# Kernel optimization log

Measured on AMD Instinct MI355X. Metric: run time of the kernel, lower is better.

The kernel has to match this reference:

```python
import jax, jax.numpy as jnp
import numpy as np

HEAD_NUM = 8
NEG_BIG = 1e9  # additive mask constant from the original layer


def setup_inputs() -> dict:
    key = jax.random.key(0)
    ks = jax.random.split(key, 7)
    B, S, D = 4, 2048, 512
    return {
        "x": jax.random.normal(ks[0], (B, S, D), dtype=jnp.float32),
        "Wk": jax.random.normal(ks[1], (D, D), dtype=jnp.float32) * (1.0 / np.sqrt(D)),
        "bk": jax.random.normal(ks[2], (D,), dtype=jnp.float32) * 0.02,
        "Wv": jax.random.normal(ks[3], (D, D), dtype=jnp.float32) * (1.0 / np.sqrt(D)),
        "bv": jax.random.normal(ks[4], (D,), dtype=jnp.float32) * 0.02,
        "Wo": jax.random.normal(ks[5], (D, D), dtype=jnp.float32) * (1.0 / np.sqrt(D)),
        "bo": jax.random.normal(ks[6], (D,), dtype=jnp.float32) * 0.02,
    }


def reference(x, Wk, bk, Wv, bv, Wo, bo):
    B, S, D = x.shape
    H = HEAD_NUM
    hd = D // H
    # Original layer: query is NOT projected; key/value are.
    q = x
    k = x @ Wk + bk
    v = x @ Wv + bv
    # split heads: [B, H, S, hd]
    qh = q.reshape(B, S, H, hd).transpose(0, 2, 1, 3)
    kh = k.reshape(B, S, H, hd).transpose(0, 2, 1, 3)
    vh = v.reshape(B, S, H, hd).transpose(0, 2, 1, 3)
    # scaled dot-product scores [B, H, S, S] (normalized=True => 1/sqrt(head_dim))
    scale = 1.0 / jnp.sqrt(jnp.asarray(hd, dtype=x.dtype))
    e = jnp.einsum("bhqd,bhkd->bhqk", qh, kh) * scale
    # history_only=True => causal additive mask
    causal = jnp.tril(jnp.ones((S, S), dtype=x.dtype))
    e = e - (1.0 - causal) * NEG_BIG
    a = jax.nn.softmax(e, axis=-1)
    out = jnp.einsum("bhqk,bhkd->bhqd", a, vh)  # [B, H, S, hd]
    out = out.transpose(0, 2, 1, 3).reshape(B, S, D)
    return out @ Wo + bo
```

## Files before the change

kernel.cpp:

```cpp
#include <hip/hip_runtime.h>
#include <stdint.h>
#include <stddef.h>

typedef short bf16x8 __attribute__((ext_vector_type(8)));
typedef float f32x4 __attribute__((ext_vector_type(4)));
typedef int i32x4 __attribute__((ext_vector_type(4)));

#define AS1 __attribute__((address_space(1)))
#define AS3 __attribute__((address_space(3)))

#define KSCALE 0.18033688011112042f
#define MFMA16(A, B, C) __builtin_amdgcn_mfma_f32_16x16x32_bf16(A, B, C, 0, 0, 0)

__device__ __forceinline__ unsigned short f2bf(float f) {
    union { float f; uint32_t u; } v; v.f = f;
    return (unsigned short)((v.u + 0x7fffu + ((v.u >> 16) & 1u)) >> 16);
}

__global__ void prep(const float* __restrict__ x, const float* __restrict__ Wk,
                     const float* __restrict__ Wv, const float* __restrict__ Wo,
                     unsigned short* __restrict__ xb, unsigned short* __restrict__ WkvT,
                     unsigned short* __restrict__ WoT) {
    __shared__ float tile[32][33];
    const int bi = blockIdx.x;
    const int tid = threadIdx.x;
    if (bi < 4096) {
        int i = bi * 256 + tid;
        float4 v = reinterpret_cast<const float4*>(x)[i];
        ushort4 o;
        o.x = f2bf(v.x); o.y = f2bf(v.y); o.z = f2bf(v.z); o.w = f2bf(v.w);
        reinterpret_cast<ushort4*>(xb)[i] = o;
    } else {
        int j = bi - 4096;
        int z = j >> 8, rem = j & 255;
        int bk = (rem >> 4) * 32, bn = (rem & 15) * 32;
        const float* W = (z == 0) ? Wk : (z == 1) ? Wv : Wo;
        unsigned short* WT = (z == 2) ? WoT : (WkvT + (size_t)z * 512 * 512);
        int tx = tid & 31, ty = tid >> 5;
#pragma unroll
        for (int r = 0; r < 32; r += 8)
            tile[ty + r][tx] = W[(size_t)(bk + ty + r) * 512 + bn + tx];
        __syncthreads();
#pragma unroll
        for (int r = 0; r < 32; r += 8)
            WT[(size_t)(bn + ty + r) * 512 + bk + tx] = f2bf(tile[tx][ty + r]);
    }
}

__global__ __launch_bounds__(256, 2) void gemmKV(const unsigned short* __restrict__ A,
                                                 const unsigned short* __restrict__ BT,
                                                 const float* __restrict__ bk,
                                                 const float* __restrict__ bv,
                                                 unsigned short* __restrict__ kbuf,
                                                 unsigned short* __restrict__ vTb) {
    __shared__ unsigned short lA[64 * 64];
    __shared__ unsigned short lB[128 * 64];
    const int tid = threadIdx.x;
    const int tile_n = blockIdx.x * 128;
    const int tile_m = blockIdx.y * 64;
    const int wid = tid >> 6, lane = tid & 63;
    const int wm = (wid >> 1) * 32, wn = (wid & 1) * 64;
    const int l16 = lane & 15, lg = lane >> 4;

    f32x4 acc[2][4];
#pragma unroll
    for (int i = 0; i < 2; ++i)
#pragma unroll
        for (int j = 0; j < 4; ++j)
            acc[i][j] = (f32x4){0.f, 0.f, 0.f, 0.f};

    const int r0 = tid >> 3;
    const int cr = tid & 7;

    for (int kt = 0; kt < 512; kt += 64) {
#pragma unroll
        for (int i = 0; i < 2; ++i) {
            int r = r0 + i * 32;
            int crs = cr ^ (r & 7);
            __builtin_amdgcn_global_load_lds((const AS1 void*)(A + (size_t)(tile_m + r) * 512 + kt + crs * 8),
                                             (AS3 void*)(&lA[(i * 256 + tid) * 8]), 16, 0, 0);
        }
#pragma unroll
        for (int i = 0; i < 4; ++i) {
            int r = r0 + i * 32;
            int crs = cr ^ (r & 7);
            __builtin_amdgcn_global_load_lds((const AS1 void*)(BT + (size_t)(tile_n + r) * 512 + kt + crs * 8),
                                             (AS3 void*)(&lB[(i * 256 + tid) * 8]), 16, 0, 0);
        }
        __syncthreads();
#pragma unroll
        for (int ks = 0; ks < 2; ++ks) {
            bf16x8 af[2], bfr[4];
#pragma unroll
            for (int f = 0; f < 2; ++f) {
                int ra = wm + f * 16 + l16;
                af[f] = *reinterpret_cast<const bf16x8*>(
                    reinterpret_cast<const char*>(lA) + ra * 128 + (((ks * 4 + lg) ^ (ra & 7)) << 4));
            }
#pragma unroll
            for (int f = 0; f < 4; ++f) {
                int rb = wn + f * 16 + l16;
                bfr[f] = *reinterpret_cast<const bf16x8*>(
                    reinterpret_cast<const char*>(lB) + rb * 128 + (((ks * 4 + lg) ^ (rb & 7)) << 4));
            }
#pragma unroll
            for (int fm = 0; fm < 2; ++fm)
#pragma unroll
                for (int fn = 0; fn < 4; ++fn)
                    acc[fm][fn] = MFMA16(af[fm], bfr[fn], acc[fm][fn]);
        }
        __syncthreads();
    }

#pragma unroll
    for (int fm = 0; fm < 2; ++fm)
#pragma unroll
        for (int fn = 0; fn < 4; ++fn) {
            int gm0 = tile_m + wm + fm * 16 + lg * 4;
            int gn = tile_n + wn + fn * 16 + l16;
            bool isK = gn < 512;
            int gnn = isK ? gn : gn - 512;
            float bs = isK ? bk[gnn] : bv[gnn];
            int hh = gnn >> 6, d = gnn & 63;
#pragma unroll
            for (int r = 0; r < 4; ++r) {
                float v = acc[fm][fn][r] + bs;
                int m = gm0 + r;
                int b = m >> 11, s = m & 2047;
                if (isK)
                    kbuf[(((size_t)(b * 8 + hh) * 2048 + s) << 6) + d] = f2bf(v * KSCALE);
                else
                    vTb[(((size_t)(b * 8 + hh) * 64 + d) << 11) + s] = f2bf(v);
            }
        }
}

__global__ __launch_bounds__(256, 2) void gemmO(const unsigned short* __restrict__ A,
                                                const unsigned short* __restrict__ BT,
                                                const float* __restrict__ bias,
                                                float* __restrict__ outp) {
    __shared__ unsigned short lA[64 * 64];
    __shared__ unsigned short lB[128 * 64];
    const int tid = threadIdx.x;
    const int tile_n = blockIdx.x * 128;
    const int tile_m = blockIdx.y * 64;
    const int wid = tid >> 6, lane = tid & 63;
    const int wm = (wid >> 1) * 32, wn = (wid & 1) * 64;
    const int l16 = lane & 15, lg = lane >> 4;

    f32x4 acc[2][4];
#pragma unroll
    for (int i = 0; i < 2; ++i)
#pragma unroll
        for (int j = 0; j < 4; ++j)
            acc[i][j] = (f32x4){0.f, 0.f, 0.f, 0.f};

    const int r0 = tid >> 3;
    const int cr = tid & 7;

    for (int kt = 0; kt < 512; kt += 64) {
#pragma unroll
        for (int i = 0; i < 2; ++i) {
            int r = r0 + i * 32;
            int crs = cr ^ (r & 7);
            __builtin_amdgcn_global_load_lds((const AS1 void*)(A + (size_t)(tile_m + r) * 512 + kt + crs * 8),
                                             (AS3 void*)(&lA[(i * 256 + tid) * 8]), 16, 0, 0);
        }
#pragma unroll
        for (int i = 0; i < 4; ++i) {
            int r = r0 + i * 32;
            int crs = cr ^ (r & 7);
            __builtin_amdgcn_global_load_lds((const AS1 void*)(BT + (size_t)(tile_n + r) * 512 + kt + crs * 8),
                                             (AS3 void*)(&lB[(i * 256 + tid) * 8]), 16, 0, 0);
        }
        __syncthreads();
#pragma unroll
        for (int ks = 0; ks < 2; ++ks) {
            bf16x8 af[2], bfr[4];
#pragma unroll
            for (int f = 0; f < 2; ++f) {
                int ra = wm + f * 16 + l16;
                af[f] = *reinterpret_cast<const bf16x8*>(
                    reinterpret_cast<const char*>(lA) + ra * 128 + (((ks * 4 + lg) ^ (ra & 7)) << 4));
            }
#pragma unroll
            for (int f = 0; f < 4; ++f) {
                int rb = wn + f * 16 + l16;
                bfr[f] = *reinterpret_cast<const bf16x8*>(
                    reinterpret_cast<const char*>(lB) + rb * 128 + (((ks * 4 + lg) ^ (rb & 7)) << 4));
            }
#pragma unroll
            for (int fm = 0; fm < 2; ++fm)
#pragma unroll
                for (int fn = 0; fn < 4; ++fn)
                    acc[fm][fn] = MFMA16(af[fm], bfr[fn], acc[fm][fn]);
        }
        __syncthreads();
    }

#pragma unroll
    for (int fm = 0; fm < 2; ++fm)
#pragma unroll
        for (int fn = 0; fn < 4; ++fn) {
            int gm0 = tile_m + wm + fm * 16 + lg * 4;
            int gn = tile_n + wn + fn * 16 + l16;
            float bs = bias[gn];
#pragma unroll
            for (int r = 0; r < 4; ++r)
                outp[(size_t)(gm0 + r) * 512 + gn] = acc[fm][fn][r] + bs;
        }
}

__global__ __launch_bounds__(256, 3) void attn_f(const unsigned short* __restrict__ xq,
                                                 const unsigned short* __restrict__ kg,
                                                 const unsigned short* __restrict__ vT,
                                                 unsigned short* __restrict__ ob) {
    __shared__ unsigned short lsK[3][4096];
    __shared__ unsigned short lsV[3][4096];

    const int tid = threadIdx.x;
    const int lane = tid & 63;
    const int w = tid >> 6;
    const int l16 = lane & 15, lg = lane >> 4;
    const int bh = blockIdx.x, b = bh >> 3, h = bh & 7;
    const int qblk = 31 - blockIdx.y;
    const int qlo = qblk * 64 + w * 16;
    const int q = qlo + l16;

    const unsigned short* Kb = kg + (size_t)bh * (2048 * 64);
    const unsigned short* Vb = vT + (size_t)bh * (64 * 2048);

    const unsigned short* qp = xq + ((size_t)(b * 2048 + qlo + l16) * 512) + h * 64 + lg * 8;
    bf16x8 qf0 = *(const bf16x8*)qp;
    bf16x8 qf1 = *(const bf16x8*)(qp + 32);

    f32x4 o[4];
#pragma unroll
    for (int i = 0; i < 4; ++i) o[i] = (f32x4){0.f, 0.f, 0.f, 0.f};
    float lsum = 0.f;

    const int nph = qblk + 1;

    const int srow = tid >> 3;
    const int scs = (tid & 7) ^ (srow & 7);
    const int skey = 8 * ((srow >> 2) & 3) + (srow & 3) + 4 * (srow >> 4);

#define STAGE(B, PH) { \
        const int kv0_ = (PH) << 6; \
        __builtin_amdgcn_global_load_lds((const AS1 void*)(Kb + (size_t)(kv0_ + skey) * 64 + scs * 8), \
            (AS3 void*)(&lsK[B][(size_t)tid * 8]), 16, 0, 0); \
        __builtin_amdgcn_global_load_lds((const AS1 void*)(Kb + (size_t)(kv0_ + 32 + skey) * 64 + scs * 8), \
            (AS3 void*)(&lsK[B][(size_t)(256 + tid) * 8]), 16, 0, 0); \
        __builtin_amdgcn_global_load_lds((const AS1 void*)(Vb + (size_t)srow * 2048 + kv0_ + scs * 8), \
            (AS3 void*)(&lsV[B][(size_t)tid * 8]), 16, 0, 0); \
        __builtin_amdgcn_global_load_lds((const AS1 void*)(Vb + (size_t)(srow + 32) * 2048 + kv0_ + scs * 8), \
            (AS3 void*)(&lsV[B][(size_t)(256 + tid) * 8]), 16, 0, 0); }

#define QKGRP(G, PA, PB, KS, KVB) { \
            const char* r0p = (KS) + (32 * (G) + l16) * 128; \
            const char* r1p = r0p + 16 * 128; \
            bf16x8 k00 = *(const bf16x8*)(r0p + ((lg ^ sw) << 4)); \
            bf16x8 k01 = *(const bf16x8*)(r0p + (((lg + 4) ^ sw) << 4)); \
            bf16x8 k10 = *(const bf16x8*)(r1p + ((lg ^ sw) << 4)); \
            bf16x8 k11 = *(const bf16x8*)(r1p + (((lg + 4) ^ sw) << 4)); \
            f32x4 sA = (f32x4){0.f,0.f,0.f,0.f}, sB = (f32x4){0.f,0.f,0.f,0.f}; \
            __builtin_amdgcn_s_setprio(1); \
            sA = MFMA16(k00, qf0, sA); \
            sA = MFMA16(k01, qf1, sA); \
            sB = MFMA16(k10, qf0, sB); \
            sB = MFMA16(k11, qf1, sB); \
            __builtin_amdgcn_s_setprio(0); \
            if ((KVB) + 32 * (G) + 31 > qlo) { \
                _Pragma("unroll") \
                for (int r = 0; r < 4; ++r) { \
                    int kidx = (KVB) + 32 * (G) + 8 * lg + r; \
                    PA[r] = __builtin_amdgcn_exp2f(kidx > q ? -1e30f : sA[r]); \
                    PB[r] = __builtin_amdgcn_exp2f(kidx + 4 > q ? -1e30f : sB[r]); \
                } \
            } else { \
                _Pragma("unroll") \
                for (int r = 0; r < 4; ++r) { \
                    PA[r] = __builtin_amdgcn_exp2f(sA[r]); \
                    PB[r] = __builtin_amdgcn_exp2f(sB[r]); \
                } \
            } }

    const int sw = l16 & 7;
    STAGE(0, 0);
    if (nph > 1) STAGE(1, 1);
    int cur = 0, st = 2;
    for (int ph = 0; ph < nph; ++ph) {
        if (ph + 2 < nph) {
            STAGE(st, ph + 2);
            asm volatile("s_waitcnt vmcnt(8)" ::: "memory");
        } else if (ph + 1 < nph) {
            asm volatile("s_waitcnt vmcnt(4)" ::: "memory");
        } else {
            asm volatile("s_waitcnt vmcnt(0)" ::: "memory");
        }
        __builtin_amdgcn_s_barrier();
        asm volatile("" ::: "memory");
        {
            const char* KS = (const char*)lsK[cur];
            const char* VS = (const char*)lsV[cur];
            const int kvb = ph << 6;
            float pA0[4], pB0[4], pA1[4], pB1[4];
            QKGRP(0, pA0, pB0, KS, kvb)
            QKGRP(1, pA1, pB1, KS, kvb)
            lsum += ((pA0[0] + pA0[1]) + (pA0[2] + pA0[3]))
                  + ((pB0[0] + pB0[1]) + (pB0[2] + pB0[3]))
                  + ((pA1[0] + pA1[1]) + (pA1[2] + pA1[3]))
                  + ((pB1[0] + pB1[1]) + (pB1[2] + pB1[3]));
            uint32_t u0, u1, u2, u3, u4, u5, u6, u7;
            asm("v_cvt_pk_bf16_f32 %0, %1, %2" : "=v"(u0) : "v"(pA0[0]), "v"(pA0[1]));
            asm("v_cvt_pk_bf16_f32 %0, %1, %2" : "=v"(u1) : "v"(pA0[2]), "v"(pA0[3]));
            asm("v_cvt_pk_bf16_f32 %0, %1, %2" : "=v"(u2) : "v"(pB0[0]), "v"(pB0[1]));
            asm("v_cvt_pk_bf16_f32 %0, %1, %2" : "=v"(u3) : "v"(pB0[2]), "v"(pB0[3]));
            asm("v_cvt_pk_bf16_f32 %0, %1, %2" : "=v"(u4) : "v"(pA1[0]), "v"(pA1[1]));
            asm("v_cvt_pk_bf16_f32 %0, %1, %2" : "=v"(u5) : "v"(pA1[2]), "v"(pA1[3]));
            asm("v_cvt_pk_bf16_f32 %0, %1, %2" : "=v"(u6) : "v"(pB1[0]), "v"(pB1[1]));
            asm("v_cvt_pk_bf16_f32 %0, %1, %2" : "=v"(u7) : "v"(pB1[2]), "v"(pB1[3]));
            union { i32x4 i; bf16x8 h; } pu0, pu1;
            pu0.i = (i32x4){(int)u0, (int)u1, (int)u2, (int)u3};
            pu1.i = (i32x4){(int)u4, (int)u5, (int)u6, (int)u7};
            __builtin_amdgcn_s_setprio(1);
#pragma unroll
            for (int nb = 0; nb < 4; ++nb) {
                const char* vr = VS + (nb * 16 + l16) * 128;
                bf16x8 vf0 = *(const bf16x8*)(vr + ((lg ^ sw) << 4));
                bf16x8 vf1 = *(const bf16x8*)(vr + (((lg + 4) ^ sw) << 4));
                o[nb] = MFMA16(pu0.h, vf0, o[nb]);
                o[nb] = MFMA16(pu1.h, vf1, o[nb]);
            }
            __builtin_amdgcn_s_setprio(0);
        }
        asm volatile("" ::: "memory");
        __builtin_amdgcn_s_barrier();
        cur = (cur == 2) ? 0 : cur + 1;
        st = (st == 2) ? 0 : st + 1;
    }
#undef STAGE
#undef QKGRP

    lsum += __shfl_xor(lsum, 16, 64);
    lsum += __shfl_xor(lsum, 32, 64);
    float linv[4];
#pragma unroll
    for (int r = 0; r < 4; ++r)
        linv[r] = 1.f / __shfl(lsum, 4 * lg + r, 64);
#pragma unroll
    for (int nb = 0; nb < 4; ++nb)
#pragma unroll
        for (int r = 0; r < 4; ++r) {
            int s = qlo + 4 * lg + r;
            ob[(size_t)(b * 2048 + s) * 512 + h * 64 + nb * 16 + l16] = f2bf(o[nb][r] * linv[r]);
        }
}

extern "C" void kernel_launch(void* const* d_in, const int* in_sizes, int n_in,
                              void* d_out, int out_size, void* d_ws, size_t ws_size,
                              hipStream_t stream) {
    const float* x  = (const float*)d_in[0];
    const float* Wk = (const float*)d_in[1];
    const float* bk = (const float*)d_in[2];
    const float* Wv = (const float*)d_in[3];
    const float* bv = (const float*)d_in[4];
    const float* Wo = (const float*)d_in[5];
    const float* bo = (const float*)d_in[6];

    char* ws = (char*)d_ws;
    unsigned short* xb    = (unsigned short*)(ws);
    unsigned short* kbuf  = (unsigned short*)(ws + (8ull << 20));
    unsigned short* vTb   = (unsigned short*)(ws + (16ull << 20));
    unsigned short* obuf  = (unsigned short*)(ws + (24ull << 20));
    unsigned short* WkvT  = (unsigned short*)(ws + (32ull << 20));
    unsigned short* WoT   = (unsigned short*)(ws + (33ull << 20));

    prep<<<4864, 256, 0, stream>>>(x, Wk, Wv, Wo, xb, WkvT, WoT);

    gemmKV<<<dim3(8, 128), 256, 0, stream>>>(xb, WkvT, bk, bv, kbuf, vTb);

    attn_f<<<dim3(32, 32), 256, 0, stream>>>(xb, kbuf, vTb, obuf);

    gemmO<<<dim3(4, 128), 256, 0, stream>>>(obuf, WoT, bo, (float*)d_out);
}
```

Baseline: 85.07 us.

## Split prep kernel, separate K/V GEMM grid by z, use MFMA for softmax row sums

The fused prep kernel becomes two launches, one converting x to bf16 and one transposing the three weight matrices. gemmKV now picks the K or V weights per blockIdx.z instead of per output column. In attention, the per-lane scalar sum of probabilities plus the final cross-lane shuffles is replaced by an extra pair of MFMAs against a vector of ones, moving the row-sum work from VALU to the matrix unit. The extra kernel launch adds overhead, and the ones-MFMA adds matrix-unit work in each phase.

```diff
diff --git a/kernel.cpp b/kernel.cpp
--- a/kernel.cpp
+++ b/kernel.cpp
@@ -17,38 +17,36 @@
     return (unsigned short)((v.u + 0x7fffu + ((v.u >> 16) & 1u)) >> 16);
 }
 
-__global__ void prep(const float* __restrict__ x, const float* __restrict__ Wk,
-                     const float* __restrict__ Wv, const float* __restrict__ Wo,
-                     unsigned short* __restrict__ xb, unsigned short* __restrict__ WkvT,
-                     unsigned short* __restrict__ WoT) {
+__global__ void cvt_f32_bf16(const float* __restrict__ in, unsigned short* __restrict__ out, int n4) {
+    int i = blockIdx.x * blockDim.x + threadIdx.x;
+    if (i >= n4) return;
+    float4 v = reinterpret_cast<const float4*>(in)[i];
+    ushort4 o;
+    o.x = f2bf(v.x); o.y = f2bf(v.y); o.z = f2bf(v.z); o.w = f2bf(v.w);
+    reinterpret_cast<ushort4*>(out)[i] = o;
+}
+
+__global__ void wtrans3(const float* __restrict__ Wk, const float* __restrict__ Wv,
+                        const float* __restrict__ Wo,
+                        unsigned short* __restrict__ WkT, unsigned short* __restrict__ WvT,
+                        unsigned short* __restrict__ WoT) {
     __shared__ float tile[32][33];
-    const int bi = blockIdx.x;
-    const int tid = threadIdx.x;
-    if (bi < 4096) {
-        int i = bi * 256 + tid;
-        float4 v = reinterpret_cast<const float4*>(x)[i];
-        ushort4 o;
-        o.x = f2bf(v.x); o.y = f2bf(v.y); o.z = f2bf(v.z); o.w = f2bf(v.w);
-        reinterpret_cast<ushort4*>(xb)[i] = o;
-    } else {
-        int j = bi - 4096;
-        int z = j >> 8, rem = j & 255;
-        int bk = (rem >> 4) * 32, bn = (rem & 15) * 32;
-        const float* W = (z == 0) ? Wk : (z == 1) ? Wv : Wo;
-        unsigned short* WT = (z == 2) ? WoT : (WkvT + (size_t)z * 512 * 512);
-        int tx = tid & 31, ty = tid >> 5;
-#pragma unroll
-        for (int r = 0; r < 32; r += 8)
-            tile[ty + r][tx] = W[(size_t)(bk + ty + r) * 512 + bn + tx];
-        __syncthreads();
-#pragma unroll
-        for (int r = 0; r < 32; r += 8)
-            WT[(size_t)(bn + ty + r) * 512 + bk + tx] = f2bf(tile[tx][ty + r]);
-    }
+    const float* W = (blockIdx.z == 0) ? Wk : (blockIdx.z == 1) ? Wv : Wo;
+    unsigned short* WT = (blockIdx.z == 0) ? WkT : (blockIdx.z == 1) ? WvT : WoT;
+    int bk = blockIdx.x * 32, bn = blockIdx.y * 32;
+    int tx = threadIdx.x, ty = threadIdx.y;
+#pragma unroll
+    for (int r = 0; r < 32; r += 8)
+        tile[ty + r][tx] = W[(size_t)(bk + ty + r) * 512 + bn + tx];
+    __syncthreads();
+#pragma unroll
+    for (int r = 0; r < 32; r += 8)
+        WT[(size_t)(bn + ty + r) * 512 + bk + tx] = f2bf(tile[tx][ty + r]);
 }
 
 __global__ __launch_bounds__(256, 2) void gemmKV(const unsigned short* __restrict__ A,
-                                                 const unsigned short* __restrict__ BT,
+                                                 const unsigned short* __restrict__ WkT,
+                                                 const unsigned short* __restrict__ WvT,
                                                  const float* __restrict__ bk,
                                                  const float* __restrict__ bv,
                                                  unsigned short* __restrict__ kbuf,
@@ -56,6 +54,9 @@
     __shared__ unsigned short lA[64 * 64];
     __shared__ unsigned short lB[128 * 64];
     const int tid = threadIdx.x;
+    const bool isK = (blockIdx.z == 0);
+    const unsigned short* BT = isK ? WkT : WvT;
+    const float* bias = isK ? bk : bv;
     const int tile_n = blockIdx.x * 128;
     const int tile_m = blockIdx.y * 64;
     const int wid = tid >> 6, lane = tid & 63;
@@ -118,10 +119,8 @@
         for (int fn = 0; fn < 4; ++fn) {
             int gm0 = tile_m + wm + fm * 16 + lg * 4;
             int gn = tile_n + wn + fn * 16 + l16;
-            bool isK = gn < 512;
-            int gnn = isK ? gn : gn - 512;
-            float bs = isK ? bk[gnn] : bv[gnn];
-            int hh = gnn >> 6, d = gnn & 63;
+            float bs = bias[gn];
+            int hh = gn >> 6, d = gn & 63;
 #pragma unroll
             for (int r = 0; r < 4; ++r) {
                 float v = acc[fm][fn][r] + bs;
@@ -234,10 +233,13 @@
     bf16x8 qf0 = *(const bf16x8*)qp;
     bf16x8 qf1 = *(const bf16x8*)(qp + 32);
 
+    const bf16x8 vones = {(short)0x3F80, (short)0x3F80, (short)0x3F80, (short)0x3F80,
+                          (short)0x3F80, (short)0x3F80, (short)0x3F80, (short)0x3F80};
+
     f32x4 o[4];
+    f32x4 osum = (f32x4){0.f, 0.f, 0.f, 0.f};
 #pragma unroll
     for (int i = 0; i < 4; ++i) o[i] = (f32x4){0.f, 0.f, 0.f, 0.f};
-    float lsum = 0.f;
 
     const int nph = qblk + 1;
 
@@ -307,10 +309,6 @@
             float pA0[4], pB0[4], pA1[4], pB1[4];
             QKGRP(0, pA0, pB0, KS, kvb)
             QKGRP(1, pA1, pB1, KS, kvb)
-            lsum += ((pA0[0] + pA0[1]) + (pA0[2] + pA0[3]))
-                  + ((pB0[0] + pB0[1]) + (pB0[2] + pB0[3]))
-                  + ((pA1[0] + pA1[1]) + (pA1[2] + pA1[3]))
-                  + ((pB1[0] + pB1[1]) + (pB1[2] + pB1[3]));
             uint32_t u0, u1, u2, u3, u4, u5, u6, u7;
             asm("v_cvt_pk_bf16_f32 %0, %1, %2" : "=v"(u0) : "v"(pA0[0]), "v"(pA0[1]));
             asm("v_cvt_pk_bf16_f32 %0, %1, %2" : "=v"(u1) : "v"(pA0[2]), "v"(pA0[3]));
@@ -324,6 +322,8 @@
             pu0.i = (i32x4){(int)u0, (int)u1, (int)u2, (int)u3};
             pu1.i = (i32x4){(int)u4, (int)u5, (int)u6, (int)u7};
             __builtin_amdgcn_s_setprio(1);
+            osum = MFMA16(pu0.h, vones, osum);
+            osum = MFMA16(pu1.h, vones, osum);
 #pragma unroll
             for (int nb = 0; nb < 4; ++nb) {
                 const char* vr = VS + (nb * 16 + l16) * 128;
@@ -342,12 +342,10 @@
 #undef STAGE
 #undef QKGRP
 
-    lsum += __shfl_xor(lsum, 16, 64);
-    lsum += __shfl_xor(lsum, 32, 64);
     float linv[4];
 #pragma unroll
     for (int r = 0; r < 4; ++r)
-        linv[r] = 1.f / __shfl(lsum, 4 * lg + r, 64);
+        linv[r] = 1.f / osum[r];
 #pragma unroll
     for (int nb = 0; nb < 4; ++nb)
 #pragma unroll
@@ -369,16 +367,18 @@
     const float* bo = (const float*)d_in[6];
 
     char* ws = (char*)d_ws;
-    unsigned short* xb    = (unsigned short*)(ws);
-    unsigned short* kbuf  = (unsigned short*)(ws + (8ull << 20));
-    unsigned short* vTb   = (unsigned short*)(ws + (16ull << 20));
-    unsigned short* obuf  = (unsigned short*)(ws + (24ull << 20));
-    unsigned short* WkvT  = (unsigned short*)(ws + (32ull << 20));
-    unsigned short* WoT   = (unsigned short*)(ws + (33ull << 20));
-
-    prep<<<4864, 256, 0, stream>>>(x, Wk, Wv, Wo, xb, WkvT, WoT);
-
-    gemmKV<<<dim3(8, 128), 256, 0, stream>>>(xb, WkvT, bk, bv, kbuf, vTb);
+    unsigned short* xb   = (unsigned short*)(ws);
+    unsigned short* kbuf = (unsigned short*)(ws + (8ull << 20));
+    unsigned short* vTb  = (unsigned short*)(ws + (16ull << 20));
+    unsigned short* obuf = (unsigned short*)(ws + (24ull << 20));
+    unsigned short* WkT  = (unsigned short*)(ws + (32ull << 20));
+    unsigned short* WvT  = (unsigned short*)(ws + (33ull << 20));
+    unsigned short* WoT  = (unsigned short*)(ws + (34ull << 20));
+
+    cvt_f32_bf16<<<4096, 256, 0, stream>>>(x, xb, 1048576);
+    wtrans3<<<dim3(16, 16, 3), dim3(32, 8), 0, stream>>>(Wk, Wv, Wo, WkT, WvT, WoT);
+
+    gemmKV<<<dim3(4, 128, 2), 256, 0, stream>>>(xb, WkT, WvT, bk, bv, kbuf, vTb);
 
     attn_f<<<dim3(32, 32), 256, 0, stream>>>(xb, kbuf, vTb, obuf);
 
```

Measured after the change: 79.67 us. 1.07x faster.
